# Optimization experiments

Measured on AMD Instinct MI355X. Metric: run time of the kernel, lower is better.

## Reference

```python
import jax, jax.numpy as jnp
import numpy as np

TEMPERATURE = 0.5
B, D = 4096, 256


def setup_inputs() -> dict:
    key = jax.random.key(0)
    k1, k2 = jax.random.split(key)
    z_i = jax.random.normal(k1, (B, D), dtype=jnp.float32)
    z_j = jax.random.normal(k2, (B, D), dtype=jnp.float32)
    return {"z_i": z_i, "z_j": z_j}


def reference(z_i, z_j):
    batch = z_i.shape[0]
    n = 2 * batch
    z = jnp.concatenate([z_i, z_j], axis=0)                      # [2B, D]
    z = z / jnp.linalg.norm(z, axis=1, keepdims=True)            # L2-normalize rows
    # cosine_similarity of unit vectors == dot product -> single GEMM
    sim = jnp.einsum('id,jd->ij', z, z) / TEMPERATURE            # [2B, 2B]
    mask = jnp.eye(n, dtype=bool)
    sim = jnp.where(mask, -jnp.inf, sim)                         # mask self-similarity
    positives = jnp.concatenate(
        [jnp.diagonal(sim, offset=batch), jnp.diagonal(sim, offset=-batch)], axis=0
    )                                                            # [2B]
    loss = -positives + jax.nn.logsumexp(sim, axis=1)            # [2B]
    return loss.mean()
```

## Files before the change

kernel.cpp:

```cpp
#include <hip/hip_runtime.h>
#include <hip/hip_bf16.h>
#include <stdint.h>
#include <stddef.h>


#define B_ROWS 4096
#define D_DIM  256
#define N_ROWS 8192
#define BM 128
#define BN 64

typedef __bf16 bf16;
typedef bf16  bf16x8  __attribute__((ext_vector_type(8)));
typedef bf16  bf16x4  __attribute__((ext_vector_type(4)));
typedef float floatx4 __attribute__((ext_vector_type(4)));

__global__ __launch_bounds__(256) void normalize_kernel(
    const float* __restrict__ z_i, const float* __restrict__ z_j,
    bf16* __restrict__ zn, float* __restrict__ sumexp) {
  const int wave = threadIdx.x >> 6;
  const int lane = threadIdx.x & 63;
  const int row  = blockIdx.x * 4 + wave;
  const float* src = (row < B_ROWS) ? (z_i + (size_t)row * D_DIM)
                                    : (z_j + (size_t)(row - B_ROWS) * D_DIM);
  float4 v = ((const float4*)src)[lane];
  float ss = v.x * v.x + v.y * v.y + v.z * v.z + v.w * v.w;
  #pragma unroll
  for (int m = 1; m < 64; m <<= 1) ss += __shfl_xor(ss, m);
  const float rn = rsqrtf(ss);
  bf16x4 o;
  o[0] = (bf16)(v.x * rn);
  o[1] = (bf16)(v.y * rn);
  o[2] = (bf16)(v.z * rn);
  o[3] = (bf16)(v.w * rn);
  ((bf16x4*)(zn + (size_t)row * D_DIM))[lane] = o;
  if (lane == 0) sumexp[row] = 0.f;
}

__global__ __launch_bounds__(256, 2) void simexp_kernel(
    const bf16* __restrict__ zn, float* __restrict__ sumexp,
    float* __restrict__ pos) {
  __shared__ __align__(16) bf16 Bs[2][BN * D_DIM];

  const int tid   = threadIdx.x;
  const int wave  = tid >> 6;
  const int lane  = tid & 63;
  const int lcol  = lane & 15;
  const int lquad = lane >> 4;
  const int wr = (wave >> 1) * 64;
  const int wc = (wave & 1) * 32;
  const int ri = blockIdx.x >> 3;
  const int cj = blockIdx.x & 7;
  const int row_base = ri * BM;
  const int niter = (cj == 7 && ri < 32) ? 10 : 8;

  auto jt64 = [&](int it) {
    return 2 * ((ri + 4 * cj + (it >> 1)) & 63) + (it & 1);
  };

  auto stageB = [&](int buf, int jt) {
    const bf16* src = zn + (size_t)jt * BN * D_DIM;
    #pragma unroll
    for (int it = 0; it < 8; ++it) {
      const int s   = it * 256 + tid;
      const int n   = s >> 5;
      const int kcs = s & 31;
      const int kc  = (kcs & 24) | ((kcs & 7) ^ (n & 7));
      __builtin_amdgcn_global_load_lds(
          (const __attribute__((address_space(1))) unsigned int*)
              (src + (size_t)n * D_DIM + kc * 8),
          (__attribute__((address_space(3))) unsigned int*)&Bs[buf][s * 8],
          16, 0, 0);
    }
  };

  stageB(0, jt64(0));

  floatx4 af[4][8];
  #pragma unroll
  for (int ti = 0; ti < 4; ++ti) {
    const bf16* arow =
        zn + (size_t)(row_base + wr + ti * 16 + lcol) * D_DIM + lquad * 8;
    #pragma unroll
    for (int kq = 0; kq < 8; ++kq)
      af[ti][kq] = *(const floatx4*)(arow + kq * 32);
  }

  float rowsum[4][4];
  #pragma unroll
  for (int ti = 0; ti < 4; ++ti)
    #pragma unroll
    for (int r = 0; r < 4; ++r) rowsum[ti][r] = 0.f;

  #pragma unroll 1
  for (int t = 0; t < niter; ++t) {
    __syncthreads();
    if (t + 1 < niter) stageB((t + 1) & 1, jt64(t + 1));

    floatx4 acc[4][2];
    #pragma unroll
    for (int ti = 0; ti < 4; ++ti)
      #pragma unroll
      for (int tj = 0; tj < 2; ++tj) acc[ti][tj] = floatx4{0.f, 0.f, 0.f, 0.f};

    const bf16* bbase = &Bs[t & 1][0];
    #pragma unroll
    for (int kq = 0; kq < 8; ++kq) {
      const int kc  = kq * 4 + lquad;
      const int kcs = (kc & 24) | ((kc & 7) ^ (lcol & 7));
      bf16x8 bfr[2];
      #pragma unroll
      for (int tj = 0; tj < 2; ++tj) {
        const int n = wc + tj * 16 + lcol;
        bfr[tj] = *(const bf16x8*)(bbase + n * D_DIM + kcs * 8);
      }
      #pragma unroll
      for (int ti = 0; ti < 4; ++ti)
        #pragma unroll
        for (int tj = 0; tj < 2; ++tj)
          acc[ti][tj] = __builtin_amdgcn_mfma_f32_16x16x32_bf16(
              __builtin_bit_cast(bf16x8, af[ti][kq]), bfr[tj], acc[ti][tj],
              0, 0, 0);
    }

    const int s    = 4 * cj + (t >> 1);
    const bool diag = (s == 0);
    const bool posT = (s == 32);
    const int jt = jt64(t);
    const int col_base = jt * BN;
    float colsum[2] = {0.f, 0.f};
    #pragma unroll
    for (int ti = 0; ti < 4; ++ti) {
      #pragma unroll
      for (int tj = 0; tj < 2; ++tj) {
        #pragma unroll
        for (int r = 0; r < 4; ++r) {
          const float v = acc[ti][tj][r];
          float e = __builtin_amdgcn_exp2f(v * 2.8853900817779268f);
          if (diag || posT) {
            const int rg = row_base + wr + ti * 16 + lquad * 4 + r;
            const int cg = col_base + wc + tj * 16 + lcol;
            if (diag && cg == rg) e = 0.f;
            if (posT && cg == rg + B_ROWS) {
              pos[rg] = 2.0f * v;
              pos[cg] = 2.0f * v;
            }
          }
          rowsum[ti][r] += e;
          colsum[tj]    += e;
        }
      }
    }

    if (!diag) {
      #pragma unroll
      for (int tj = 0; tj < 2; ++tj) {
        float cs = colsum[tj];
        cs += __shfl_xor(cs, 16);
        cs += __shfl_xor(cs, 32);
        if (lquad == 0)
          atomicAdd(&sumexp[col_base + wc + tj * 16 + lcol], cs);
      }
    }
  }

  #pragma unroll
  for (int ti = 0; ti < 4; ++ti) {
    #pragma unroll
    for (int r = 0; r < 4; ++r) {
      float s2 = rowsum[ti][r];
      s2 += __shfl_xor(s2, 1);
      s2 += __shfl_xor(s2, 2);
      s2 += __shfl_xor(s2, 4);
      s2 += __shfl_xor(s2, 8);
      if (lcol == 0) {
        const int grow = row_base + wr + ti * 16 + lquad * 4 + r;
        atomicAdd(&sumexp[grow], s2);
      }
    }
  }
}

__global__ __launch_bounds__(1024) void reduce_kernel(
    const float* __restrict__ sumexp, const float* __restrict__ pos,
    float* __restrict__ out) {
  __shared__ float ws[16];
  const int tid = threadIdx.x;
  float s = 0.f;
  const float ln2 = 0.6931471805599453f;
  for (int k = tid; k < N_ROWS; k += 1024)
    s += __builtin_amdgcn_logf(sumexp[k]) * ln2 - pos[k];
  #pragma unroll
  for (int m = 1; m < 64; m <<= 1) s += __shfl_xor(s, m);
  const int wave = tid >> 6, lane = tid & 63;
  if (lane == 0) ws[wave] = s;
  __syncthreads();
  if (wave == 0) {
    float t = (lane < 16) ? ws[lane] : 0.f;
    #pragma unroll
    for (int m = 1; m < 16; m <<= 1) t += __shfl_xor(t, m);
    if (lane == 0) out[0] = t * (1.0f / N_ROWS);
  }
}

extern "C" void kernel_launch(void* const* d_in, const int* in_sizes, int n_in,
                              void* d_out, int out_size, void* d_ws,
                              size_t ws_size, hipStream_t stream) {
  const float* z_i = (const float*)d_in[0];
  const float* z_j = (const float*)d_in[1];
  float* out = (float*)d_out;

  bf16* zn = (bf16*)d_ws;
  float* sumexp = (float*)((char*)d_ws + (size_t)N_ROWS * D_DIM * sizeof(bf16));
  float* pos = sumexp + N_ROWS;

  normalize_kernel<<<N_ROWS / 4, 256, 0, stream>>>(z_i, z_j, zn, sumexp);
  simexp_kernel<<<512, 256, 0, stream>>>(zn, sumexp, pos);
  reduce_kernel<<<1, 1024, 0, stream>>>(sumexp, pos, out);
}
```

Baseline: 100.1 us.

## Load B tiles directly from global into registers, dropping LDS staging

Removes the double-buffered LDS staging of B tiles (global_load_lds plus __syncthreads) and has each wave load its B fragments straight from global memory into registers. A four-deep register prefetch is interleaved with the MFMA groups to hide latency. The half-tile assignment for the positive-diagonal block is also reorganized, so cj 6 and 7 each take one extra half tile (9 iterations instead of 10 for cj 7). This removes LDS traffic and barriers, but every B element is now fetched redundantly by each wave through L2/L1 and there is more register pressure.

```diff
diff --git a/kernel.cpp b/kernel.cpp
--- a/kernel.cpp
+++ b/kernel.cpp
@@ -40,8 +40,6 @@
 __global__ __launch_bounds__(256, 2) void simexp_kernel(
     const bf16* __restrict__ zn, float* __restrict__ sumexp,
     float* __restrict__ pos) {
-  __shared__ __align__(16) bf16 Bs[2][BN * D_DIM];
-
   const int tid   = threadIdx.x;
   const int wave  = tid >> 6;
   const int lane  = tid & 63;
@@ -52,29 +50,7 @@
   const int ri = blockIdx.x >> 3;
   const int cj = blockIdx.x & 7;
   const int row_base = ri * BM;
-  const int niter = (cj == 7 && ri < 32) ? 10 : 8;
-
-  auto jt64 = [&](int it) {
-    return 2 * ((ri + 4 * cj + (it >> 1)) & 63) + (it & 1);
-  };
-
-  auto stageB = [&](int buf, int jt) {
-    const bf16* src = zn + (size_t)jt * BN * D_DIM;
-    #pragma unroll
-    for (int it = 0; it < 8; ++it) {
-      const int s   = it * 256 + tid;
-      const int n   = s >> 5;
-      const int kcs = s & 31;
-      const int kc  = (kcs & 24) | ((kcs & 7) ^ (n & 7));
-      __builtin_amdgcn_global_load_lds(
-          (const __attribute__((address_space(1))) unsigned int*)
-              (src + (size_t)n * D_DIM + kc * 8),
-          (__attribute__((address_space(3))) unsigned int*)&Bs[buf][s * 8],
-          16, 0, 0);
-    }
-  };
-
-  stageB(0, jt64(0));
+  const int niter = (ri < 32 && cj >= 6) ? 9 : 8;
 
   floatx4 af[4][8];
   #pragma unroll
@@ -94,8 +70,13 @@
 
   #pragma unroll 1
   for (int t = 0; t < niter; ++t) {
-    __syncthreads();
-    if (t + 1 < niter) stageB((t + 1) & 1, jt64(t + 1));
+    const int s   = (t == 8) ? 32 : 4 * cj + (t >> 1);
+    const int sub = (t == 8) ? (cj - 6) : (t & 1);
+    const int jt  = 2 * ((ri + s) & 63) + sub;
+    const bf16* bb = zn + (size_t)jt * BN * D_DIM + lquad * 8;
+
+#define LDB(KQ, TJ) \
+    (*(const bf16x8*)(bb + (size_t)(wc + (TJ)*16 + lcol) * D_DIM + (KQ)*32))
 
     floatx4 acc[4][2];
     #pragma unroll
@@ -103,30 +84,38 @@
       #pragma unroll
       for (int tj = 0; tj < 2; ++tj) acc[ti][tj] = floatx4{0.f, 0.f, 0.f, 0.f};
 
-    const bf16* bbase = &Bs[t & 1][0];
-    #pragma unroll
-    for (int kq = 0; kq < 8; ++kq) {
-      const int kc  = kq * 4 + lquad;
-      const int kcs = (kc & 24) | ((kc & 7) ^ (lcol & 7));
-      bf16x8 bfr[2];
-      #pragma unroll
-      for (int tj = 0; tj < 2; ++tj) {
-        const int n = wc + tj * 16 + lcol;
-        bfr[tj] = *(const bf16x8*)(bbase + n * D_DIM + kcs * 8);
-      }
-      #pragma unroll
-      for (int ti = 0; ti < 4; ++ti)
-        #pragma unroll
-        for (int tj = 0; tj < 2; ++tj)
-          acc[ti][tj] = __builtin_amdgcn_mfma_f32_16x16x32_bf16(
-              __builtin_bit_cast(bf16x8, af[ti][kq]), bfr[tj], acc[ti][tj],
-              0, 0, 0);
-    }
-
-    const int s    = 4 * cj + (t >> 1);
+    bf16x8 p0[2], p1[2], p2[2], p3[2];
+    p0[0] = LDB(0, 0); p0[1] = LDB(0, 1);
+    p1[0] = LDB(1, 0); p1[1] = LDB(1, 1);
+    p2[0] = LDB(2, 0); p2[1] = LDB(2, 1);
+    p3[0] = LDB(3, 0); p3[1] = LDB(3, 1);
+
+#define MFQ(P, KQ)                                                          \
+    {                                                                       \
+      _Pragma("unroll")                                                     \
+      for (int ti = 0; ti < 4; ++ti) {                                      \
+        acc[ti][0] = __builtin_amdgcn_mfma_f32_16x16x32_bf16(               \
+            __builtin_bit_cast(bf16x8, af[ti][KQ]), P[0], acc[ti][0],       \
+            0, 0, 0);                                                       \
+        acc[ti][1] = __builtin_amdgcn_mfma_f32_16x16x32_bf16(               \
+            __builtin_bit_cast(bf16x8, af[ti][KQ]), P[1], acc[ti][1],       \
+            0, 0, 0);                                                       \
+      }                                                                     \
+    }
+
+    MFQ(p0, 0) p0[0] = LDB(4, 0); p0[1] = LDB(4, 1);
+    MFQ(p1, 1) p1[0] = LDB(5, 0); p1[1] = LDB(5, 1);
+    MFQ(p2, 2) p2[0] = LDB(6, 0); p2[1] = LDB(6, 1);
+    MFQ(p3, 3) p3[0] = LDB(7, 0); p3[1] = LDB(7, 1);
+    MFQ(p0, 4)
+    MFQ(p1, 5)
+    MFQ(p2, 6)
+    MFQ(p3, 7)
+#undef MFQ
+#undef LDB
+
     const bool diag = (s == 0);
     const bool posT = (s == 32);
-    const int jt = jt64(t);
     const int col_base = jt * BN;
     float colsum[2] = {0.f, 0.f};
     #pragma unroll
```

Result: slower. 108.5 us (+8.4%).

## Fold temperature scale into normalization, stage A tile via LDS, rebalance tile schedule

Applied to the files above, without the earlier changes.

The normalization now scales rows by sqrt(2/ln2), so the dot product directly gives the log2-domain logit and the per-element multiply before exp2 is removed. Positives are rescaled by ln2 at the few places they are written. The A fragments are loaded through LDS with the swizzled async load instead of strided global reads, which adds extra barriers at kernel start. The uneven 10-iteration blocks are split into two 9-iteration blocks to balance load. The extra scale in bf16 slightly changes rounding.

```diff
diff --git a/kernel.cpp b/kernel.cpp
--- a/kernel.cpp
+++ b/kernel.cpp
@@ -27,7 +27,7 @@
   float ss = v.x * v.x + v.y * v.y + v.z * v.z + v.w * v.w;
   #pragma unroll
   for (int m = 1; m < 64; m <<= 1) ss += __shfl_xor(ss, m);
-  const float rn = rsqrtf(ss);
+  const float rn = rsqrtf(ss) * 1.6986436f;
   bf16x4 o;
   o[0] = (bf16)(v.x * rn);
   o[1] = (bf16)(v.y * rn);
@@ -52,14 +52,15 @@
   const int ri = blockIdx.x >> 3;
   const int cj = blockIdx.x & 7;
   const int row_base = ri * BM;
-  const int niter = (cj == 7 && ri < 32) ? 10 : 8;
-
-  auto jt64 = [&](int it) {
-    return 2 * ((ri + 4 * cj + (it >> 1)) & 63) + (it & 1);
+  const int niter = (ri < 32 && cj >= 6) ? 9 : 8;
+
+  auto jt64 = [&](int t) {
+    const int s   = (t == 8) ? 32 : 4 * cj + (t >> 1);
+    const int sub = (t == 8) ? (cj - 6) : (t & 1);
+    return 2 * ((ri + s) & 63) + sub;
   };
 
-  auto stageB = [&](int buf, int jt) {
-    const bf16* src = zn + (size_t)jt * BN * D_DIM;
+  auto stage = [&](int buf, const bf16* src) {
     #pragma unroll
     for (int it = 0; it < 8; ++it) {
       const int s   = it * 256 + tid;
@@ -74,17 +75,27 @@
     }
   };
 
-  stageB(0, jt64(0));
+  stage(0, zn + (size_t)row_base * D_DIM);
+  stage(1, zn + (size_t)(row_base + 64) * D_DIM);
+  __syncthreads();
 
   floatx4 af[4][8];
-  #pragma unroll
-  for (int ti = 0; ti < 4; ++ti) {
-    const bf16* arow =
-        zn + (size_t)(row_base + wr + ti * 16 + lcol) * D_DIM + lquad * 8;
-    #pragma unroll
-    for (int kq = 0; kq < 8; ++kq)
-      af[ti][kq] = *(const floatx4*)(arow + kq * 32);
-  }
+  {
+    const int half = wr >> 6;
+    #pragma unroll
+    for (int ti = 0; ti < 4; ++ti) {
+      const int n = ti * 16 + lcol;
+      #pragma unroll
+      for (int kq = 0; kq < 8; ++kq) {
+        const int kc  = kq * 4 + lquad;
+        const int kcs = (kc & 24) | ((kc & 7) ^ (n & 7));
+        af[ti][kq] = *(const floatx4*)(&Bs[half][(n * 32 + kcs) * 8]);
+      }
+    }
+  }
+  __syncthreads();
+
+  stage(0, zn + (size_t)jt64(0) * BN * D_DIM);
 
   float rowsum[4][4];
   #pragma unroll
@@ -95,7 +106,7 @@
   #pragma unroll 1
   for (int t = 0; t < niter; ++t) {
     __syncthreads();
-    if (t + 1 < niter) stageB((t + 1) & 1, jt64(t + 1));
+    if (t + 1 < niter) stage((t + 1) & 1, zn + (size_t)jt64(t + 1) * BN * D_DIM);
 
     floatx4 acc[4][2];
     #pragma unroll
@@ -107,11 +118,11 @@
     #pragma unroll
     for (int kq = 0; kq < 8; ++kq) {
       const int kc  = kq * 4 + lquad;
-      const int kcs = (kc & 24) | ((kc & 7) ^ (lcol & 7));
       bf16x8 bfr[2];
       #pragma unroll
       for (int tj = 0; tj < 2; ++tj) {
-        const int n = wc + tj * 16 + lcol;
+        const int n   = wc + tj * 16 + lcol;
+        const int kcs = (kc & 24) | ((kc & 7) ^ (n & 7));
         bfr[tj] = *(const bf16x8*)(bbase + n * D_DIM + kcs * 8);
       }
       #pragma unroll
@@ -123,7 +134,7 @@
               0, 0, 0);
     }
 
-    const int s    = 4 * cj + (t >> 1);
+    const int s    = (t == 8) ? 32 : 4 * cj + (t >> 1);
     const bool diag = (s == 0);
     const bool posT = (s == 32);
     const int jt = jt64(t);
@@ -136,14 +147,15 @@
         #pragma unroll
         for (int r = 0; r < 4; ++r) {
           const float v = acc[ti][tj][r];
-          float e = __builtin_amdgcn_exp2f(v * 2.8853900817779268f);
+          float e = __builtin_amdgcn_exp2f(v);
           if (diag || posT) {
             const int rg = row_base + wr + ti * 16 + lquad * 4 + r;
             const int cg = col_base + wc + tj * 16 + lcol;
             if (diag && cg == rg) e = 0.f;
             if (posT && cg == rg + B_ROWS) {
-              pos[rg] = 2.0f * v;
-              pos[cg] = 2.0f * v;
+              const float p = v * 0.6931471805599453f;
+              pos[rg] = p;
+              pos[cg] = p;
             }
           }
           rowsum[ti][r] += e;
```

Result: faster. 95.57 us (-4.5%).
